# Kernel tuning notes

Hardware: AMD Instinct MI355X
Metric: run time of the kernel (lower is better)

Reference implementation:

```python
import jax, jax.numpy as jnp
import numpy as np

DIM = 768
NUM_HEADS = 12
HEAD_DIM = DIM // NUM_HEADS
SCALE = HEAD_DIM ** -0.5


def setup_inputs() -> dict:
    key = jax.random.key(0)
    k1, k2, k3, k4 = jax.random.split(key, 4)
    B, N = 4, 2048
    x = jax.random.normal(k1, (B, N, DIM), dtype=jnp.float32)
    # torch Linear(dim, 3*dim, bias=False): weight [3*dim, dim]
    w_qkv = jax.random.normal(k2, (3 * DIM, DIM), dtype=jnp.float32) * (DIM ** -0.5)
    # proj: Linear(dim, dim) with bias
    w_proj = jax.random.normal(k3, (DIM, DIM), dtype=jnp.float32) * (DIM ** -0.5)
    b_proj = jax.random.normal(k4, (DIM,), dtype=jnp.float32) * 0.01
    return {"x": x, "w_qkv": w_qkv, "w_proj": w_proj, "b_proj": b_proj}


def reference(x, w_qkv, w_proj, b_proj):
    B, N, D = x.shape
    H, Hd = NUM_HEADS, HEAD_DIM
    qkv = x @ w_qkv.T                              # [B, N, 3D]
    qkv = qkv.reshape(B, N, 3, H, Hd)
    qkv = jnp.transpose(qkv, (2, 0, 3, 1, 4))      # [3, B, H, N, Hd]
    q, k, v = qkv[0], qkv[1], qkv[2]
    attn = jnp.einsum('bhnd,bhmd->bhnm', q, k) * SCALE  # [B, H, N, N]
    attn = jax.nn.softmax(attn, axis=-1)
    out = jnp.einsum('bhnm,bhmd->bhnd', attn, v)   # [B, H, N, Hd]
    out = jnp.transpose(out, (0, 2, 1, 3)).reshape(B, N, D)
    return out @ w_proj.T + b_proj
```

## Files before the change

### kernel.cpp

```cpp
#include <hip/hip_runtime.h>
#include <hip/hip_bf16.h>

#define DIM      768
#define NHEADS   12
#define HEADDIM  64
#define BATCH    4
#define SEQ      2048
#define NROWS    (BATCH * SEQ)
#define QKVCOLS  (3 * DIM)
#define SLOT     ((size_t)BATCH * NHEADS * SEQ * HEADDIM)

#define QSCALE_LOG2 0.18033688011112042f

typedef short bf16x8_t __attribute__((ext_vector_type(8)));
typedef short bf16x4_t __attribute__((ext_vector_type(4)));
typedef float f32x4_t  __attribute__((ext_vector_type(4)));

__device__ __forceinline__ short f2bf(float f) {
    union { __hip_bfloat16 h; short s; } u;
    u.h = __float2bfloat16(f);
    return u.s;
}

__device__ __forceinline__ bf16x4_t cvt4(float4 v) {
    bf16x4_t o;
    o[0] = f2bf(v.x); o[1] = f2bf(v.y); o[2] = f2bf(v.z); o[3] = f2bf(v.w);
    return o;
}

__device__ __forceinline__ float exp2_fast(float x) {
#if __has_builtin(__builtin_amdgcn_exp2f)
    return __builtin_amdgcn_exp2f(x);
#else
    return __expf(x * 0.6931471805599453f);
#endif
}

__global__ __launch_bounds__(256) void qkv_gemm(const float* __restrict__ X,
                                                const float* __restrict__ W,
                                                __hip_bfloat16* __restrict__ QKV) {
    __shared__ __hip_bfloat16 lds[128 * 72 + 64 * 72];
    __hip_bfloat16* As = lds;
    __hip_bfloat16* Bs = lds + 128 * 72;

    const int tid  = threadIdx.x;
    const int wave = tid >> 6;
    const int lane = tid & 63;
    const int quad = lane >> 4;
    const int l16  = lane & 15;
    const int m0   = blockIdx.x * 128;
    const int n0   = blockIdx.y * 64;

    f32x4_t acc[2][4];
#pragma unroll
    for (int i = 0; i < 2; i++)
#pragma unroll
        for (int j = 0; j < 4; j++) acc[i][j] = (f32x4_t){0.f, 0.f, 0.f, 0.f};

    for (int k0 = 0; k0 < 768; k0 += 64) {
        __syncthreads();
#pragma unroll
        for (int i = 0; i < 8; i++) {
            int c = tid + i * 256;
            int r = c >> 4, c4 = (c & 15) << 2;
            float4 v = *(const float4*)(X + (size_t)(m0 + r) * 768 + k0 + c4);
            *(bf16x4_t*)(As + r * 72 + c4) = cvt4(v);
        }
#pragma unroll
        for (int i = 0; i < 4; i++) {
            int c = tid + i * 256;
            int r = c >> 4, c4 = (c & 15) << 2;
            float4 v = *(const float4*)(W + (size_t)(n0 + r) * 768 + k0 + c4);
            *(bf16x4_t*)(Bs + r * 72 + c4) = cvt4(v);
        }
        __syncthreads();

        const int mrow = wave * 32;
#pragma unroll
        for (int kc = 0; kc < 2; kc++) {
            bf16x8_t a0 = *(const bf16x8_t*)(As + (mrow + l16) * 72 + kc * 32 + quad * 8);
            bf16x8_t a1 = *(const bf16x8_t*)(As + (mrow + 16 + l16) * 72 + kc * 32 + quad * 8);
#pragma unroll
            for (int nt = 0; nt < 4; nt++) {
                bf16x8_t b = *(const bf16x8_t*)(Bs + (nt * 16 + l16) * 72 + kc * 32 + quad * 8);
                acc[0][nt] = __builtin_amdgcn_mfma_f32_16x16x32_bf16(a0, b, acc[0][nt], 0, 0, 0);
                acc[1][nt] = __builtin_amdgcn_mfma_f32_16x16x32_bf16(a1, b, acc[1][nt], 0, 0, 0);
            }
        }
    }

    const int bidx  = m0 >> 11;
    const int nbase = (m0 & 2047) + wave * 32;
#pragma unroll
    for (int ms = 0; ms < 2; ms++) {
#pragma unroll
        for (int nt = 0; nt < 4; nt++) {
            int col   = n0 + nt * 16 + l16;
            int which = col / 768;
            int rem   = col - which * 768;
            int h     = rem >> 6;
            int d     = rem & 63;
            if (which == 2) {
                size_t base = 2 * SLOT + (((size_t)bidx * NHEADS + h) * HEADDIM + d) * SEQ
                            + nbase + ms * 16 + quad * 4;
                bf16x4_t pk;
#pragma unroll
                for (int r = 0; r < 4; r++) pk[r] = f2bf(acc[ms][nt][r]);
                *(bf16x4_t*)(QKV + base) = pk;
            } else {
                float sc = (which == 0) ? QSCALE_LOG2 : 1.0f;
                size_t rowbase = ((size_t)bidx * NHEADS + h) * SEQ;
                size_t slotoff = (size_t)which * SLOT;
#pragma unroll
                for (int r = 0; r < 4; r++) {
                    int n = nbase + ms * 16 + quad * 4 + r;
                    QKV[slotoff + (rowbase + n) * HEADDIM + d] =
                        __float2bfloat16(acc[ms][nt][r] * sc);
                }
            }
        }
    }
}

__global__ __launch_bounds__(512) void attn(const __hip_bfloat16* __restrict__ QKV,
                                            __hip_bfloat16* __restrict__ ATT) {
    __shared__ __hip_bfloat16 lds[384 * 72];
    __hip_bfloat16* Qs = lds;
    __hip_bfloat16* Ks = lds + 128 * 72;
    __hip_bfloat16* Vs = lds + 256 * 72;

    const int tid  = threadIdx.x;
    const int wave = tid >> 6;
    const int lane = tid & 63;
    const int quad = lane >> 4;
    const int l16  = lane & 15;
    const int qb   = blockIdx.x;
    const int bh   = blockIdx.y;
    const int b    = bh / NHEADS;
    const int h    = bh - b * NHEADS;

    const __hip_bfloat16* Qg = QKV + 0 * SLOT + (((size_t)b * NHEADS + h) * SEQ) * HEADDIM;
    const __hip_bfloat16* Kg = QKV + 1 * SLOT + (((size_t)b * NHEADS + h) * SEQ) * HEADDIM;
    const __hip_bfloat16* Vg = QKV + 2 * SLOT + (((size_t)b * NHEADS + h) * HEADDIM) * SEQ;

    const int rs = tid >> 3;
    const int es = (tid & 7) * 8;

#pragma unroll
    for (int i = 0; i < 2; i++) {
        int c = tid + i * 512;
        int r = c >> 3, e = (c & 7) * 8;
        *(bf16x8_t*)(Qs + r * 72 + e) =
            *(const bf16x8_t*)(Qg + (size_t)(qb * 128 + r) * HEADDIM + e);
    }
    *(bf16x8_t*)(Ks + rs * 72 + es) = *(const bf16x8_t*)(Kg + (size_t)rs * HEADDIM + es);
    *(bf16x8_t*)(Vs + rs * 72 + es) = *(const bf16x8_t*)(Vg + (size_t)rs * SEQ + es);
    __syncthreads();

    bf16x8_t aq[2];
#pragma unroll
    for (int kc = 0; kc < 2; kc++)
        aq[kc] = *(const bf16x8_t*)(Qs + (wave * 16 + l16) * 72 + kc * 32 + quad * 8);

    __hip_bfloat16* Pw = Qs + wave * 16 * 72;

    f32x4_t o[4];
#pragma unroll
    for (int dt = 0; dt < 4; dt++) o[dt] = (f32x4_t){0.f, 0.f, 0.f, 0.f};
    float l_i[4] = {0.f, 0.f, 0.f, 0.f};

    for (int t = 0; t < SEQ / 64; t++) {
        const int cur = t & 1;
        __hip_bfloat16* Kc = Ks + cur * 64 * 72;
        __hip_bfloat16* Vc = Vs + cur * 64 * 72;

        bf16x8_t nk, nv;
        const bool has_next = (t + 1 < SEQ / 64);
        if (has_next) {
            int n0 = (t + 1) * 64;
            nk = *(const bf16x8_t*)(Kg + (size_t)(n0 + rs) * HEADDIM + es);
            nv = *(const bf16x8_t*)(Vg + (size_t)rs * SEQ + n0 + es);
        }

        f32x4_t s[4];
#pragma unroll
        for (int nt = 0; nt < 4; nt++) {
            s[nt] = (f32x4_t){0.f, 0.f, 0.f, 0.f};
#pragma unroll
            for (int kc = 0; kc < 2; kc++) {
                bf16x8_t bk = *(const bf16x8_t*)(Kc + (nt * 16 + l16) * 72 + kc * 32 + quad * 8);
                s[nt] = __builtin_amdgcn_mfma_f32_16x16x32_bf16(aq[kc], bk, s[nt], 0, 0, 0);
            }
        }

#pragma unroll
        for (int nt = 0; nt < 4; nt++)
#pragma unroll
            for (int r = 0; r < 4; r++) {
                float p = exp2_fast(s[nt][r]);
                s[nt][r] = p;
                l_i[r] += p;
            }

#pragma unroll
        for (int nt = 0; nt < 4; nt++)
#pragma unroll
            for (int r = 0; r < 4; r++)
                Pw[(quad * 4 + r) * 72 + nt * 16 + l16] = __float2bfloat16(s[nt][r]);

#pragma unroll
        for (int kc = 0; kc < 2; kc++) {
            bf16x8_t ap = *(const bf16x8_t*)(Pw + l16 * 72 + kc * 32 + quad * 8);
#pragma unroll
            for (int dt = 0; dt < 4; dt++) {
                bf16x8_t bv = *(const bf16x8_t*)(Vc + (dt * 16 + l16) * 72 + kc * 32 + quad * 8);
                o[dt] = __builtin_amdgcn_mfma_f32_16x16x32_bf16(ap, bv, o[dt], 0, 0, 0);
            }
        }

        if (has_next) {
            __hip_bfloat16* Kn = Ks + (1 - cur) * 64 * 72;
            __hip_bfloat16* Vn = Vs + (1 - cur) * 64 * 72;
            *(bf16x8_t*)(Kn + rs * 72 + es) = nk;
            *(bf16x8_t*)(Vn + rs * 72 + es) = nv;
        }
        __syncthreads();
    }

#pragma unroll
    for (int msk = 1; msk < 16; msk <<= 1)
#pragma unroll
        for (int r = 0; r < 4; r++) l_i[r] += __shfl_xor(l_i[r], msk, 16);

#pragma unroll
    for (int dt = 0; dt < 4; dt++) {
#pragma unroll
        for (int r = 0; r < 4; r++) {
            int n = qb * 128 + wave * 16 + quad * 4 + r;
            int d = dt * 16 + l16;
            float val = o[dt][r] / l_i[r];
            ATT[((size_t)b * SEQ + n) * DIM + h * HEADDIM + d] = __float2bfloat16(val);
        }
    }
}

__global__ __launch_bounds__(256) void proj_gemm(const __hip_bfloat16* __restrict__ A,
                                                 const float* __restrict__ W,
                                                 const float* __restrict__ bias,
                                                 float* __restrict__ OUT) {
    __shared__ __hip_bfloat16 lds[128 * 72 + 64 * 72];
    __hip_bfloat16* As = lds;
    __hip_bfloat16* Bs = lds + 128 * 72;

    const int tid  = threadIdx.x;
    const int wave = tid >> 6;
    const int lane = tid & 63;
    const int quad = lane >> 4;
    const int l16  = lane & 15;
    const int m0   = blockIdx.x * 128;
    const int n0   = blockIdx.y * 64;

    f32x4_t acc[2][4];
#pragma unroll
    for (int i = 0; i < 2; i++)
#pragma unroll
        for (int j = 0; j < 4; j++) acc[i][j] = (f32x4_t){0.f, 0.f, 0.f, 0.f};

    for (int k0 = 0; k0 < 768; k0 += 64) {
        __syncthreads();
#pragma unroll
        for (int i = 0; i < 4; i++) {
            int c = tid + i * 256;
            int r = c >> 3, e = (c & 7) * 8;
            *(bf16x8_t*)(As + r * 72 + e) =
                *(const bf16x8_t*)(A + (size_t)(m0 + r) * 768 + k0 + e);
        }
#pragma unroll
        for (int i = 0; i < 4; i++) {
            int c = tid + i * 256;
            int r = c >> 4, c4 = (c & 15) << 2;
            float4 v = *(const float4*)(W + (size_t)(n0 + r) * 768 + k0 + c4);
            *(bf16x4_t*)(Bs + r * 72 + c4) = cvt4(v);
        }
        __syncthreads();

        const int mrow = wave * 32;
#pragma unroll
        for (int kc = 0; kc < 2; kc++) {
            bf16x8_t a0 = *(const bf16x8_t*)(As + (mrow + l16) * 72 + kc * 32 + quad * 8);
            bf16x8_t a1 = *(const bf16x8_t*)(As + (mrow + 16 + l16) * 72 + kc * 32 + quad * 8);
#pragma unroll
            for (int nt = 0; nt < 4; nt++) {
                bf16x8_t b = *(const bf16x8_t*)(Bs + (nt * 16 + l16) * 72 + kc * 32 + quad * 8);
                acc[0][nt] = __builtin_amdgcn_mfma_f32_16x16x32_bf16(a0, b, acc[0][nt], 0, 0, 0);
                acc[1][nt] = __builtin_amdgcn_mfma_f32_16x16x32_bf16(a1, b, acc[1][nt], 0, 0, 0);
            }
        }
    }

#pragma unroll
    for (int ms = 0; ms < 2; ms++) {
#pragma unroll
        for (int nt = 0; nt < 4; nt++) {
            int col = n0 + nt * 16 + l16;
            float bv = bias[col];
#pragma unroll
            for (int r = 0; r < 4; r++) {
                int row = m0 + wave * 32 + ms * 16 + quad * 4 + r;
                OUT[(size_t)row * 768 + col] = acc[ms][nt][r] + bv;
            }
        }
    }
}

extern "C" void kernel_launch(void* const* d_in, const int* in_sizes, int n_in,
                              void* d_out, int out_size, void* d_ws, size_t ws_size,
                              hipStream_t stream) {
    const float* x      = (const float*)d_in[0];
    const float* w_qkv  = (const float*)d_in[1];
    const float* w_proj = (const float*)d_in[2];
    const float* b_proj = (const float*)d_in[3];
    float* out = (float*)d_out;

    __hip_bfloat16* qkv_ws = (__hip_bfloat16*)d_ws;
    __hip_bfloat16* att_ws = qkv_ws + 3 * SLOT;

    dim3 g1(NROWS / 128, QKVCOLS / 64);
    qkv_gemm<<<g1, 256, 0, stream>>>(x, w_qkv, qkv_ws);

    dim3 g2(SEQ / 128, BATCH * NHEADS);
    attn<<<g2, 512, 0, stream>>>(qkv_ws, att_ws);

    dim3 g3(NROWS / 128, DIM / 64);
    proj_gemm<<<g3, 256, 0, stream>>>(att_ws, w_proj, b_proj, out);
}
```

Before: 244.0 us.

## Pre-convert inputs to bf16 and use direct-to-LDS loads with larger swizzled GEMM tiles

Adds a conversion kernel that turns x and both weight matrices into bf16 in the workspace before the GEMMs. Both GEMMs are rebuilt around a shared macro that uses global_load_lds 16-byte staging with an XOR-swizzled LDS layout and a 128x128 tile, with each wave computing a 64x64 sub-tile. This removes per-tile fp32 loads and conversions inside the GEMMs and raises data reuse per block. The cost is an extra kernel launch plus a full read and write pass over x and the weights, and the x buffer is reused as the attention output buffer.

```diff
diff --git a/kernel.cpp b/kernel.cpp
--- a/kernel.cpp
+++ b/kernel.cpp
@@ -22,12 +22,6 @@
     return u.s;
 }
 
-__device__ __forceinline__ bf16x4_t cvt4(float4 v) {
-    bf16x4_t o;
-    o[0] = f2bf(v.x); o[1] = f2bf(v.y); o[2] = f2bf(v.z); o[3] = f2bf(v.w);
-    return o;
-}
-
 __device__ __forceinline__ float exp2_fast(float x) {
 #if __has_builtin(__builtin_amdgcn_exp2f)
     return __builtin_amdgcn_exp2f(x);
@@ -36,86 +30,116 @@
 #endif
 }
 
-__global__ __launch_bounds__(256) void qkv_gemm(const float* __restrict__ X,
-                                                const float* __restrict__ W,
+__device__ __forceinline__ void stage16(const __hip_bfloat16* g, __hip_bfloat16* l) {
+    __builtin_amdgcn_global_load_lds(
+        (const __attribute__((address_space(1))) void*)g,
+        (__attribute__((address_space(3))) void*)l,
+        16, 0, 0);
+}
+
+#define NX8  ((size_t)NROWS * DIM / 8)
+#define NWQ8 ((size_t)QKVCOLS * DIM / 8)
+#define NWP8 ((size_t)DIM * DIM / 8)
+
+__global__ __launch_bounds__(256) void cvt_all(const float* __restrict__ X,
+                                               const float* __restrict__ Wq,
+                                               const float* __restrict__ Wp,
+                                               __hip_bfloat16* __restrict__ Xb,
+                                               __hip_bfloat16* __restrict__ Wqb,
+                                               __hip_bfloat16* __restrict__ Wpb) {
+    size_t i = (size_t)blockIdx.x * 256 + threadIdx.x;
+    const float* src; __hip_bfloat16* dst; size_t off;
+    if (i < NX8)                  { src = X;  dst = Xb;  off = i; }
+    else if (i < NX8 + NWQ8)      { src = Wq; dst = Wqb; off = i - NX8; }
+    else                          { src = Wp; dst = Wpb; off = i - NX8 - NWQ8; }
+    float4 a = ((const float4*)src)[off * 2];
+    float4 b = ((const float4*)src)[off * 2 + 1];
+    bf16x8_t o;
+    o[0] = f2bf(a.x); o[1] = f2bf(a.y); o[2] = f2bf(a.z); o[3] = f2bf(a.w);
+    o[4] = f2bf(b.x); o[5] = f2bf(b.y); o[6] = f2bf(b.z); o[7] = f2bf(b.w);
+    *(bf16x8_t*)(dst + off * 8) = o;
+}
+
+#define GEMM_CORE(Aptr, Bptr)                                                   \
+    __shared__ __hip_bfloat16 As[128 * 64];                                     \
+    __shared__ __hip_bfloat16 Bs[128 * 64];                                     \
+    const int tid  = threadIdx.x;                                               \
+    const int wave = tid >> 6;                                                  \
+    const int lane = tid & 63;                                                  \
+    const int quad = lane >> 4;                                                 \
+    const int l16  = lane & 15;                                                 \
+    const int wm   = wave >> 1;                                                 \
+    const int wn   = wave & 1;                                                  \
+    const int m0   = blockIdx.x * 128;                                          \
+    const int n0   = blockIdx.y * 128;                                          \
+    const int sr   = lane >> 3;                     \
+    const int sc   = ((lane & 7) ^ sr) * 8;         \
+    f32x4_t acc[4][4];                                                          \
+    _Pragma("unroll")                                                           \
+    for (int i = 0; i < 4; i++)                                                 \
+        _Pragma("unroll")                                                       \
+        for (int j = 0; j < 4; j++) acc[i][j] = (f32x4_t){0.f, 0.f, 0.f, 0.f};  \
+    for (int k0 = 0; k0 < 768; k0 += 64) {                                      \
+        __syncthreads();                                                        \
+        _Pragma("unroll")                                                       \
+        for (int i = 0; i < 4; i++) {                                           \
+            int seg = wave * 4 + i;                                  \
+            int row = seg * 8 + sr;                                             \
+            stage16(Aptr + (size_t)(m0 + row) * 768 + k0 + sc, As + seg * 512); \
+            stage16(Bptr + (size_t)(n0 + row) * 768 + k0 + sc, Bs + seg * 512); \
+        }                                                                       \
+        __syncthreads();               \
+        _Pragma("unroll")                                                       \
+        for (int kc = 0; kc < 2; kc++) {                                        \
+            const int dsw = ((kc * 4 + quad) ^ (l16 & 7)) * 8;                  \
+            bf16x8_t af[4], bfr[4];                                             \
+            _Pragma("unroll")                                                   \
+            for (int mt = 0; mt < 4; mt++)                                      \
+                af[mt] = *(const bf16x8_t*)(As + (wm * 64 + mt * 16 + l16) * 64 + dsw); \
+            _Pragma("unroll")                                                   \
+            for (int nt = 0; nt < 4; nt++)                                      \
+                bfr[nt] = *(const bf16x8_t*)(Bs + (wn * 64 + nt * 16 + l16) * 64 + dsw); \
+            _Pragma("unroll")                                                   \
+            for (int mt = 0; mt < 4; mt++)                                      \
+                _Pragma("unroll")                                               \
+                for (int nt = 0; nt < 4; nt++)                                  \
+                    acc[mt][nt] = __builtin_amdgcn_mfma_f32_16x16x32_bf16(      \
+                        af[mt], bfr[nt], acc[mt][nt], 0, 0, 0);                 \
+        }                                                                       \
+    }
+
+__global__ __launch_bounds__(256) void qkv_gemm(const __hip_bfloat16* __restrict__ Xb,
+                                                const __hip_bfloat16* __restrict__ Wqb,
                                                 __hip_bfloat16* __restrict__ QKV) {
-    __shared__ __hip_bfloat16 lds[128 * 72 + 64 * 72];
-    __hip_bfloat16* As = lds;
-    __hip_bfloat16* Bs = lds + 128 * 72;
-
-    const int tid  = threadIdx.x;
-    const int wave = tid >> 6;
-    const int lane = tid & 63;
-    const int quad = lane >> 4;
-    const int l16  = lane & 15;
-    const int m0   = blockIdx.x * 128;
-    const int n0   = blockIdx.y * 64;
-
-    f32x4_t acc[2][4];
-#pragma unroll
-    for (int i = 0; i < 2; i++)
-#pragma unroll
-        for (int j = 0; j < 4; j++) acc[i][j] = (f32x4_t){0.f, 0.f, 0.f, 0.f};
-
-    for (int k0 = 0; k0 < 768; k0 += 64) {
-        __syncthreads();
-#pragma unroll
-        for (int i = 0; i < 8; i++) {
-            int c = tid + i * 256;
-            int r = c >> 4, c4 = (c & 15) << 2;
-            float4 v = *(const float4*)(X + (size_t)(m0 + r) * 768 + k0 + c4);
-            *(bf16x4_t*)(As + r * 72 + c4) = cvt4(v);
-        }
-#pragma unroll
-        for (int i = 0; i < 4; i++) {
-            int c = tid + i * 256;
-            int r = c >> 4, c4 = (c & 15) << 2;
-            float4 v = *(const float4*)(W + (size_t)(n0 + r) * 768 + k0 + c4);
-            *(bf16x4_t*)(Bs + r * 72 + c4) = cvt4(v);
-        }
-        __syncthreads();
-
-        const int mrow = wave * 32;
-#pragma unroll
-        for (int kc = 0; kc < 2; kc++) {
-            bf16x8_t a0 = *(const bf16x8_t*)(As + (mrow + l16) * 72 + kc * 32 + quad * 8);
-            bf16x8_t a1 = *(const bf16x8_t*)(As + (mrow + 16 + l16) * 72 + kc * 32 + quad * 8);
-#pragma unroll
-            for (int nt = 0; nt < 4; nt++) {
-                bf16x8_t b = *(const bf16x8_t*)(Bs + (nt * 16 + l16) * 72 + kc * 32 + quad * 8);
-                acc[0][nt] = __builtin_amdgcn_mfma_f32_16x16x32_bf16(a0, b, acc[0][nt], 0, 0, 0);
-                acc[1][nt] = __builtin_amdgcn_mfma_f32_16x16x32_bf16(a1, b, acc[1][nt], 0, 0, 0);
-            }
-        }
-    }
-
-    const int bidx  = m0 >> 11;
-    const int nbase = (m0 & 2047) + wave * 32;
-#pragma unroll
-    for (int ms = 0; ms < 2; ms++) {
+    GEMM_CORE(Xb, Wqb)
+
+    const int bidx = m0 >> 11;
+    const int seqb = (m0 & 2047) + wm * 64;
+#pragma unroll
+    for (int mt = 0; mt < 4; mt++) {
 #pragma unroll
         for (int nt = 0; nt < 4; nt++) {
-            int col   = n0 + nt * 16 + l16;
+            int col   = n0 + wn * 64 + nt * 16 + l16;
             int which = col / 768;
             int rem   = col - which * 768;
             int h     = rem >> 6;
             int d     = rem & 63;
             if (which == 2) {
                 size_t base = 2 * SLOT + (((size_t)bidx * NHEADS + h) * HEADDIM + d) * SEQ
-                            + nbase + ms * 16 + quad * 4;
+                            + seqb + mt * 16 + quad * 4;
                 bf16x4_t pk;
 #pragma unroll
-                for (int r = 0; r < 4; r++) pk[r] = f2bf(acc[ms][nt][r]);
+                for (int r = 0; r < 4; r++) pk[r] = f2bf(acc[mt][nt][r]);
                 *(bf16x4_t*)(QKV + base) = pk;
             } else {
-                float sc = (which == 0) ? QSCALE_LOG2 : 1.0f;
+                float sc2 = (which == 0) ? QSCALE_LOG2 : 1.0f;
                 size_t rowbase = ((size_t)bidx * NHEADS + h) * SEQ;
                 size_t slotoff = (size_t)which * SLOT;
 #pragma unroll
                 for (int r = 0; r < 4; r++) {
-                    int n = nbase + ms * 16 + quad * 4 + r;
+                    int n = seqb + mt * 16 + quad * 4 + r;
                     QKV[slotoff + (rowbase + n) * HEADDIM + d] =
-                        __float2bfloat16(acc[ms][nt][r] * sc);
+                        __float2bfloat16(acc[mt][nt][r] * sc2);
                 }
             }
         }
@@ -245,69 +269,21 @@
 }
 
 __global__ __launch_bounds__(256) void proj_gemm(const __hip_bfloat16* __restrict__ A,
-                                                 const float* __restrict__ W,
+                                                 const __hip_bfloat16* __restrict__ B,
                                                  const float* __restrict__ bias,
                                                  float* __restrict__ OUT) {
-    __shared__ __hip_bfloat16 lds[128 * 72 + 64 * 72];
-    __hip_bfloat16* As = lds;
-    __hip_bfloat16* Bs = lds + 128 * 72;
-
-    const int tid  = threadIdx.x;
-    const int wave = tid >> 6;
-    const int lane = tid & 63;
-    const int quad = lane >> 4;
-    const int l16  = lane & 15;
-    const int m0   = blockIdx.x * 128;
-    const int n0   = blockIdx.y * 64;
-
-    f32x4_t acc[2][4];
-#pragma unroll
-    for (int i = 0; i < 2; i++)
-#pragma unroll
-        for (int j = 0; j < 4; j++) acc[i][j] = (f32x4_t){0.f, 0.f, 0.f, 0.f};
-
-    for (int k0 = 0; k0 < 768; k0 += 64) {
-        __syncthreads();
-#pragma unroll
-        for (int i = 0; i < 4; i++) {
-            int c = tid + i * 256;
-            int r = c >> 3, e = (c & 7) * 8;
-            *(bf16x8_t*)(As + r * 72 + e) =
-                *(const bf16x8_t*)(A + (size_t)(m0 + r) * 768 + k0 + e);
-        }
-#pragma unroll
-        for (int i = 0; i < 4; i++) {
-            int c = tid + i * 256;
-            int r = c >> 4, c4 = (c & 15) << 2;
-            float4 v = *(const float4*)(W + (size_t)(n0 + r) * 768 + k0 + c4);
-            *(bf16x4_t*)(Bs + r * 72 + c4) = cvt4(v);
-        }
-        __syncthreads();
-
-        const int mrow = wave * 32;
-#pragma unroll
-        for (int kc = 0; kc < 2; kc++) {
-            bf16x8_t a0 = *(const bf16x8_t*)(As + (mrow + l16) * 72 + kc * 32 + quad * 8);
-            bf16x8_t a1 = *(const bf16x8_t*)(As + (mrow + 16 + l16) * 72 + kc * 32 + quad * 8);
-#pragma unroll
-            for (int nt = 0; nt < 4; nt++) {
-                bf16x8_t b = *(const bf16x8_t*)(Bs + (nt * 16 + l16) * 72 + kc * 32 + quad * 8);
-                acc[0][nt] = __builtin_amdgcn_mfma_f32_16x16x32_bf16(a0, b, acc[0][nt], 0, 0, 0);
-                acc[1][nt] = __builtin_amdgcn_mfma_f32_16x16x32_bf16(a1, b, acc[1][nt], 0, 0, 0);
-            }
-        }
-    }
-
-#pragma unroll
-    for (int ms = 0; ms < 2; ms++) {
+    GEMM_CORE(A, B)
+
+#pragma unroll
+    for (int mt = 0; mt < 4; mt++) {
 #pragma unroll
         for (int nt = 0; nt < 4; nt++) {
-            int col = n0 + nt * 16 + l16;
+            int col = n0 + wn * 64 + nt * 16 + l16;
             float bv = bias[col];
 #pragma unroll
             for (int r = 0; r < 4; r++) {
-                int row = m0 + wave * 32 + ms * 16 + quad * 4 + r;
-                OUT[(size_t)row * 768 + col] = acc[ms][nt][r] + bv;
+                int row = m0 + wm * 64 + mt * 16 + quad * 4 + r;
+                OUT[(size_t)row * 768 + col] = acc[mt][nt][r] + bv;
             }
         }
     }
@@ -323,14 +299,20 @@
     float* out = (float*)d_out;
 
     __hip_bfloat16* qkv_ws = (__hip_bfloat16*)d_ws;
-    __hip_bfloat16* att_ws = qkv_ws + 3 * SLOT;
-
-    dim3 g1(NROWS / 128, QKVCOLS / 64);
-    qkv_gemm<<<g1, 256, 0, stream>>>(x, w_qkv, qkv_ws);
+    __hip_bfloat16* xb     = qkv_ws + 3 * SLOT;
+    __hip_bfloat16* att_ws = xb;
+    __hip_bfloat16* wqb    = xb + (size_t)NROWS * DIM;
+    __hip_bfloat16* wpb    = wqb + (size_t)QKVCOLS * DIM;
+
+    int cvt_blocks = (int)((NX8 + NWQ8 + NWP8) / 256);
+    cvt_all<<<cvt_blocks, 256, 0, stream>>>(x, w_qkv, w_proj, xb, wqb, wpb);
+
+    dim3 g1(NROWS / 128, QKVCOLS / 128);
+    qkv_gemm<<<g1, 256, 0, stream>>>(xb, wqb, qkv_ws);
 
     dim3 g2(SEQ / 128, BATCH * NHEADS);
     attn<<<g2, 512, 0, stream>>>(qkv_ws, att_ws);
 
-    dim3 g3(NROWS / 128, DIM / 64);
-    proj_gemm<<<g3, 256, 0, stream>>>(att_ws, w_proj, b_proj, out);
-}
+    dim3 g3(NROWS / 128, DIM / 128);
+    proj_gemm<<<g3, 256, 0, stream>>>(att_ws, wpb, b_proj, out);
+}
```

New measurement: 236.3 us. 3.1% less time.
